# Performance work log

Hardware: AMD Instinct MI355X
Metric: run time of the kernel (lower is better)

The kernel has to match this reference:

```python
import jax, jax.numpy as jnp
import numpy as np

N_NODES = 50000
N_EDGES = 800000
IN_FEATS = 256
OUT_FEATS = 64


def setup_inputs() -> dict:
    key = jax.random.key(0)
    k1, k2, k3, k4, k5 = jax.random.split(key, 5)
    feat = jax.random.normal(k1, (N_NODES, IN_FEATS), dtype=jnp.float32)
    weight = jax.random.normal(k2, (OUT_FEATS, IN_FEATS), dtype=jnp.float32) * (1.0 / np.sqrt(IN_FEATS))
    bias = jax.random.normal(k3, (OUT_FEATS,), dtype=jnp.float32) * 0.01
    src = jax.random.randint(k4, (N_EDGES,), 0, N_NODES, dtype=jnp.int32)
    dst = jax.random.randint(k5, (N_EDGES,), 0, N_NODES, dtype=jnp.int32)
    return {"feat": feat, "weight": weight, "bias": bias, "src": src, "dst": dst}


def reference(feat, weight, bias, src, dst):
    # GCN conv, norm='both', in_feats > out_feats branch:
    #   feat := feat * out_deg^{-1/2}; h := feat @ W^T (Qlinear); rst := SpMM(copy_u,sum);
    #   rst := rst * in_deg^{-1/2} + bias
    n = feat.shape[0]
    ones = jnp.ones(src.shape, dtype=jnp.float32)
    out_deg = jnp.clip(jax.ops.segment_sum(ones, src, num_segments=n), 1.0)  # [N]
    in_deg = jnp.clip(jax.ops.segment_sum(ones, dst, num_segments=n), 1.0)   # [N]

    h = feat * jax.lax.rsqrt(out_deg)[:, None]          # left norm
    h = jnp.einsum('ni,oi->no', h, weight)              # [N, out] quantized linear (fp math)
    msg = jnp.take(h, src, axis=0)                      # gather: copy_u, [E, out]
    rst = jax.ops.segment_sum(msg, dst, num_segments=n) # scatter-sum, [N, out]
    rst = rst * jax.lax.rsqrt(in_deg)[:, None]          # right norm
    rst = rst + bias
    return rst
```

## Files before the change

### kernel.cpp

```cpp
#include <hip/hip_runtime.h>
#include <hip/hip_bf16.h>


#define IN_F 256
#define OUT_F 64
#define CAP 64

typedef short bf16x8 __attribute__((ext_vector_type(8)));
typedef float f32x4 __attribute__((ext_vector_type(4)));
typedef unsigned short u16x8 __attribute__((ext_vector_type(8)));

static __host__ __device__ inline size_t ws_align(size_t x) { return (x + 15) & ~(size_t)15; }

__device__ inline unsigned short f2bf(float x) {
  unsigned u = __float_as_uint(x);
  unsigned r = (u + 0x7fffu + ((u >> 16) & 1u)) >> 16;
  return (unsigned short)r;
}
__device__ inline float bf2f(unsigned short b) { return __uint_as_float(((unsigned)b) << 16); }

__global__ void wsplit_kernel(const float* __restrict__ W, unsigned short* __restrict__ whi,
                              unsigned short* __restrict__ wlo, int total) {
  int i = blockIdx.x * blockDim.x + threadIdx.x;
  if (i < total) {
    float x = W[i];
    unsigned short hb = f2bf(x);
    whi[i] = hb;
    wlo[i] = f2bf(x - bf2f(hb));
  }
}

__global__ __launch_bounds__(256) void fused_kernel(const float* __restrict__ feat,
                                                    const unsigned short* __restrict__ whi,
                                                    const unsigned short* __restrict__ wlo,
                                                    const int* __restrict__ src,
                                                    const int* __restrict__ dst,
                                                    int* __restrict__ outcnt,
                                                    int* __restrict__ cursor,
                                                    unsigned short* __restrict__ csr,
                                                    float* __restrict__ h,
                                                    int n, int E, int gemmBlocks) {
  if ((int)blockIdx.x >= gemmBlocks) {
    int e = ((int)blockIdx.x - gemmBlocks) * 256 + threadIdx.x;
    if (e < E) {
      int s = src[e], d = dst[e];
      atomicAdd(&outcnt[s], 1);
      int p = atomicAdd(&cursor[d], 1);
      csr[(size_t)d * CAP + p] = (unsigned short)s;
    }
    return;
  }
  const int tid = threadIdx.x;
  const int wave = tid >> 6;
  const int lane = tid & 63;
  const int lrow = lane & 15;
  const int kgrp = lane >> 4;
  const int base = blockIdx.x * 64 + wave * 16;

  f32x4 acc[4] = {};

  int anode = base + lrow;
  if (anode >= n) anode = n - 1;
  const float* ap = feat + (size_t)anode * IN_F + kgrp * 8;
  const int wofs = lrow * IN_F + kgrp * 8;

#pragma unroll 2
  for (int k0 = 0; k0 < IN_F; k0 += 32) {
    float4 a0 = *(const float4*)(ap + k0);
    float4 a1 = *(const float4*)(ap + k0 + 4);
    float av[8] = {a0.x, a0.y, a0.z, a0.w, a1.x, a1.y, a1.z, a1.w};
    bf16x8 fhi, flo;
#pragma unroll
    for (int j = 0; j < 8; ++j) {
      unsigned short hb = f2bf(av[j]);
      fhi[j] = (short)hb;
      flo[j] = (short)f2bf(av[j] - bf2f(hb));
    }
#pragma unroll
    for (int oj = 0; oj < 4; ++oj) {
      const int bofs = oj * 16 * IN_F + wofs + k0;
      bf16x8 bhi = *(const bf16x8*)(whi + bofs);
      bf16x8 blo = *(const bf16x8*)(wlo + bofs);
      acc[oj] = __builtin_amdgcn_mfma_f32_16x16x32_bf16(fhi, bhi, acc[oj], 0, 0, 0);
      acc[oj] = __builtin_amdgcn_mfma_f32_16x16x32_bf16(fhi, blo, acc[oj], 0, 0, 0);
      acc[oj] = __builtin_amdgcn_mfma_f32_16x16x32_bf16(flo, bhi, acc[oj], 0, 0, 0);
    }
  }

#pragma unroll
  for (int r = 0; r < 4; ++r) {
    int node = base + kgrp * 4 + r;
    if (node < n) {
#pragma unroll
      for (int oj = 0; oj < 4; ++oj) {
        h[(size_t)node * OUT_F + oj * 16 + lrow] = acc[oj][r];
      }
    }
  }
}

__global__ __launch_bounds__(256) void gather_kernel(const float* __restrict__ h,
                                                     const int* __restrict__ cursor,
                                                     const int* __restrict__ outcnt,
                                                     const unsigned short* __restrict__ csr,
                                                     const float* __restrict__ bias,
                                                     float* __restrict__ out, int n) {
  int node = (blockIdx.x * blockDim.x + threadIdx.x) >> 6;
  int lane = threadIdx.x & 63;
  if (node >= n) return;
  int cnt = cursor[node];
  const unsigned short* bp = csr + (size_t)node * CAP;
  float acc = 0.f;
  int p = 0;
  for (; p + 8 <= cnt; p += 8) {
    u16x8 v = *(const u16x8*)(bp + p);
    int s0 = v[0], s1 = v[1], s2 = v[2], s3 = v[3];
    int s4 = v[4], s5 = v[5], s6 = v[6], s7 = v[7];
    float r0 = 1.0f / sqrtf(fmaxf((float)outcnt[s0], 1.0f));
    float r1 = 1.0f / sqrtf(fmaxf((float)outcnt[s1], 1.0f));
    float r2 = 1.0f / sqrtf(fmaxf((float)outcnt[s2], 1.0f));
    float r3 = 1.0f / sqrtf(fmaxf((float)outcnt[s3], 1.0f));
    float r4 = 1.0f / sqrtf(fmaxf((float)outcnt[s4], 1.0f));
    float r5 = 1.0f / sqrtf(fmaxf((float)outcnt[s5], 1.0f));
    float r6 = 1.0f / sqrtf(fmaxf((float)outcnt[s6], 1.0f));
    float r7 = 1.0f / sqrtf(fmaxf((float)outcnt[s7], 1.0f));
    float a0 = h[(size_t)s0 * OUT_F + lane], a1 = h[(size_t)s1 * OUT_F + lane];
    float a2 = h[(size_t)s2 * OUT_F + lane], a3 = h[(size_t)s3 * OUT_F + lane];
    float a4 = h[(size_t)s4 * OUT_F + lane], a5 = h[(size_t)s5 * OUT_F + lane];
    float a6 = h[(size_t)s6 * OUT_F + lane], a7 = h[(size_t)s7 * OUT_F + lane];
    acc += ((a0 * r0 + a1 * r1) + (a2 * r2 + a3 * r3)) +
           ((a4 * r4 + a5 * r5) + (a6 * r6 + a7 * r7));
  }
  for (; p < cnt; ++p) {
    int s = bp[p];
    float r = 1.0f / sqrtf(fmaxf((float)outcnt[s], 1.0f));
    acc += h[(size_t)s * OUT_F + lane] * r;
  }
  float rs = 1.0f / sqrtf(fmaxf((float)cnt, 1.0f));
  out[(size_t)node * OUT_F + lane] = acc * rs + bias[lane];
}

extern "C" void kernel_launch(void* const* d_in, const int* in_sizes, int n_in,
                              void* d_out, int out_size, void* d_ws, size_t ws_size,
                              hipStream_t stream) {
  const float* feat = (const float*)d_in[0];
  const float* W    = (const float*)d_in[1];
  const float* bias = (const float*)d_in[2];
  const int* src    = (const int*)d_in[3];
  const int* dst    = (const int*)d_in[4];
  float* out = (float*)d_out;

  const int N = in_sizes[0] / IN_F;
  const int E = in_sizes[3];
  const int WTOT = OUT_F * IN_F;

  size_t o_outcnt = 0;
  size_t o_cursor = o_outcnt + ws_align(N);
  size_t o_csr    = o_cursor + ws_align(N);
  size_t o_whi    = o_csr + ws_align((size_t)N * CAP / 2);
  size_t o_wlo    = o_whi + ws_align(WTOT / 2);
  size_t o_h      = o_wlo + ws_align(WTOT / 2);

  int* outcnt  = (int*)d_ws + o_outcnt;
  int* cursor  = (int*)d_ws + o_cursor;
  unsigned short* csr = (unsigned short*)((int*)d_ws + o_csr);
  unsigned short* whi = (unsigned short*)((int*)d_ws + o_whi);
  unsigned short* wlo = (unsigned short*)((int*)d_ws + o_wlo);
  float* h     = (float*)d_ws + o_h;

  hipMemsetAsync(d_ws, 0, o_csr * sizeof(int), stream);

  const int gemmBlocks = (N + 63) / 64;
  const int fillBlocks = (E + 255) / 256;
  wsplit_kernel<<<(WTOT + 255) / 256, 256, 0, stream>>>(W, whi, wlo, WTOT);
  fused_kernel<<<gemmBlocks + fillBlocks, 256, 0, stream>>>(feat, whi, wlo, src, dst,
                                                            outcnt, cursor, csr, h,
                                                            N, E, gemmBlocks);
  gather_kernel<<<(N + 3) / 4, 256, 0, stream>>>(h, cursor, outcnt, csr, bias, out, N);
}
```

Before: 231.6 us.

## Fold workspace zeroing into weight split kernel and deepen gather unrolling

Replaces the hipMemsetAsync of the degree counters with zeroing done inside the weight-split kernel, removing one stream operation. The h store in the GEMM becomes nontemporal. The gather loop gets a 16-wide unrolled stage to put more independent loads in flight. Reciprocal square roots now use __frsqrt_rn instead of a divide by sqrtf. The nontemporal store may hurt, since h is read back right away by the gather kernel.

```diff
diff --git a/kernel.cpp b/kernel.cpp
--- a/kernel.cpp
+++ b/kernel.cpp
@@ -20,14 +20,16 @@
 __device__ inline float bf2f(unsigned short b) { return __uint_as_float(((unsigned)b) << 16); }
 
 __global__ void wsplit_kernel(const float* __restrict__ W, unsigned short* __restrict__ whi,
-                              unsigned short* __restrict__ wlo, int total) {
+                              unsigned short* __restrict__ wlo, int wtot,
+                              int* __restrict__ zbase, int zcount) {
   int i = blockIdx.x * blockDim.x + threadIdx.x;
-  if (i < total) {
+  if (i < wtot) {
     float x = W[i];
     unsigned short hb = f2bf(x);
     whi[i] = hb;
     wlo[i] = f2bf(x - bf2f(hb));
   }
+  if (i < zcount) zbase[i] = 0;
 }
 
 __global__ __launch_bounds__(256) void fused_kernel(const float* __restrict__ feat,
@@ -93,7 +95,7 @@
     if (node < n) {
 #pragma unroll
       for (int oj = 0; oj < 4; ++oj) {
-        h[(size_t)node * OUT_F + oj * 16 + lrow] = acc[oj][r];
+        __builtin_nontemporal_store(acc[oj][r], &h[(size_t)node * OUT_F + oj * 16 + lrow]);
       }
     }
   }
@@ -112,31 +114,42 @@
   const unsigned short* bp = csr + (size_t)node * CAP;
   float acc = 0.f;
   int p = 0;
+  for (; p + 16 <= cnt; p += 16) {
+    u16x8 v0 = *(const u16x8*)(bp + p);
+    u16x8 v1 = *(const u16x8*)(bp + p + 8);
+    float a[16], r[16];
+#pragma unroll
+    for (int j = 0; j < 8; ++j) {
+      int s = v0[j];
+      a[j] = h[(size_t)s * OUT_F + lane];
+      r[j] = __frsqrt_rn(fmaxf((float)outcnt[s], 1.0f));
+    }
+#pragma unroll
+    for (int j = 0; j < 8; ++j) {
+      int s = v1[j];
+      a[8 + j] = h[(size_t)s * OUT_F + lane];
+      r[8 + j] = __frsqrt_rn(fmaxf((float)outcnt[s], 1.0f));
+    }
+    float t0 = 0.f, t1 = 0.f;
+#pragma unroll
+    for (int j = 0; j < 8; ++j) { t0 += a[j] * r[j]; t1 += a[8 + j] * r[8 + j]; }
+    acc += t0 + t1;
+  }
   for (; p + 8 <= cnt; p += 8) {
     u16x8 v = *(const u16x8*)(bp + p);
-    int s0 = v[0], s1 = v[1], s2 = v[2], s3 = v[3];
-    int s4 = v[4], s5 = v[5], s6 = v[6], s7 = v[7];
-    float r0 = 1.0f / sqrtf(fmaxf((float)outcnt[s0], 1.0f));
-    float r1 = 1.0f / sqrtf(fmaxf((float)outcnt[s1], 1.0f));
-    float r2 = 1.0f / sqrtf(fmaxf((float)outcnt[s2], 1.0f));
-    float r3 = 1.0f / sqrtf(fmaxf((float)outcnt[s3], 1.0f));
-    float r4 = 1.0f / sqrtf(fmaxf((float)outcnt[s4], 1.0f));
-    float r5 = 1.0f / sqrtf(fmaxf((float)outcnt[s5], 1.0f));
-    float r6 = 1.0f / sqrtf(fmaxf((float)outcnt[s6], 1.0f));
-    float r7 = 1.0f / sqrtf(fmaxf((float)outcnt[s7], 1.0f));
-    float a0 = h[(size_t)s0 * OUT_F + lane], a1 = h[(size_t)s1 * OUT_F + lane];
-    float a2 = h[(size_t)s2 * OUT_F + lane], a3 = h[(size_t)s3 * OUT_F + lane];
-    float a4 = h[(size_t)s4 * OUT_F + lane], a5 = h[(size_t)s5 * OUT_F + lane];
-    float a6 = h[(size_t)s6 * OUT_F + lane], a7 = h[(size_t)s7 * OUT_F + lane];
-    acc += ((a0 * r0 + a1 * r1) + (a2 * r2 + a3 * r3)) +
-           ((a4 * r4 + a5 * r5) + (a6 * r6 + a7 * r7));
+    float t = 0.f;
+#pragma unroll
+    for (int j = 0; j < 8; ++j) {
+      int s = v[j];
+      t += h[(size_t)s * OUT_F + lane] * __frsqrt_rn(fmaxf((float)outcnt[s], 1.0f));
+    }
+    acc += t;
   }
   for (; p < cnt; ++p) {
     int s = bp[p];
-    float r = 1.0f / sqrtf(fmaxf((float)outcnt[s], 1.0f));
-    acc += h[(size_t)s * OUT_F + lane] * r;
+    acc += h[(size_t)s * OUT_F + lane] * __frsqrt_rn(fmaxf((float)outcnt[s], 1.0f));
   }
-  float rs = 1.0f / sqrtf(fmaxf((float)cnt, 1.0f));
+  float rs = __frsqrt_rn(fmaxf((float)cnt, 1.0f));
   out[(size_t)node * OUT_F + lane] = acc * rs + bias[lane];
 }
 
@@ -168,11 +181,13 @@
   unsigned short* wlo = (unsigned short*)((int*)d_ws + o_wlo);
   float* h     = (float*)d_ws + o_h;
 
-  hipMemsetAsync(d_ws, 0, o_csr * sizeof(int), stream);
+  const int zcount = (int)o_csr;
+  const int wzmax = zcount > WTOT ? zcount : WTOT;
 
   const int gemmBlocks = (N + 63) / 64;
   const int fillBlocks = (E + 255) / 256;
-  wsplit_kernel<<<(WTOT + 255) / 256, 256, 0, stream>>>(W, whi, wlo, WTOT);
+  wsplit_kernel<<<(wzmax + 255) / 256, 256, 0, stream>>>(W, whi, wlo, WTOT,
+                                                         (int*)d_ws, zcount);
   fused_kernel<<<gemmBlocks + fillBlocks, 256, 0, stream>>>(feat, whi, wlo, src, dst,
                                                             outcnt, cursor, csr, h,
                                                             N, E, gemmBlocks);
```

After: 219.7 us. -5.2%, faster.
